# Performance work log

Hardware: AMD Instinct MI355X
Metric: run time of the kernel (lower is better)

Reference implementation:

```python
import jax, jax.numpy as jnp
import numpy as np

DIM = 128      # d_model (C)
DEPTH = 8
D_INNER = 2 * DIM      # expand=2
D_STATE = 16
D_CONV = 4
DT_RANK = (DIM + 15) // 16  # ceil(d_model/16) = 8
EPS = 1e-6
B_SZ, H_SZ, W_SZ = 2, 64, 64


def setup_inputs() -> dict:
    key = jax.random.key(0)
    ks = jax.random.split(key, 8)
    s = 0.02
    f32 = jnp.float32
    inp = {
        "x": jax.random.normal(ks[0], (B_SZ, DIM, H_SZ, W_SZ), f32),
        "in_proj_w": (jax.random.normal(ks[1], (DEPTH, 2 * D_INNER, DIM), f32) * s),
        "conv_w": (jax.random.normal(ks[2], (DEPTH, D_INNER, D_CONV), f32) * s),
        "conv_b": jnp.zeros((DEPTH, D_INNER), f32),
        "x_proj_w": (jax.random.normal(ks[3], (DEPTH, DT_RANK + 2 * D_STATE, D_INNER), f32) * s),
        "dt_proj_w": (jax.random.normal(ks[4], (DEPTH, D_INNER, DT_RANK), f32) * s),
        "dt_proj_b": jax.random.uniform(ks[5], (DEPTH, D_INNER), f32, -4.0, -2.0),
        "A_log": jnp.tile(jnp.log(jnp.arange(1.0, D_STATE + 1.0, dtype=f32))[None, None, :], (DEPTH, D_INNER, 1)),
        "D_skip": jnp.ones((DEPTH, D_INNER), f32),
        "out_proj_w": (jax.random.normal(ks[6], (DEPTH, DIM, D_INNER), f32) * s),
        "rms_w": jnp.ones((DIM,), f32),
    }
    return inp


def _selective_scan(u, delta, A, Bm, Cm, D_skip):
    # u, delta: [B,L,Dn]; A: [Dn,N]; Bm, Cm: [B,L,N]; D_skip: [Dn]
    dA = jnp.exp(delta[..., None] * A)                      # [B,L,Dn,N]
    dBu = (delta * u)[..., None] * Bm[:, :, None, :]        # [B,L,Dn,N]
    def comb(c1, c2):
        a1, b1 = c1
        a2, b2 = c2
        return a1 * a2, a2 * b1 + b2
    _, h = jax.lax.associative_scan(comb, (dA, dBu), axis=1)  # h: [B,L,Dn,N]
    y = jnp.einsum('bldn,bln->bld', h, Cm) + u * D_skip
    return y


def _mamba_layer(x, in_w, cw, cb, xp_w, dtw, dtb, A_log, D_skip, out_w):
    # x: [B,L,D]
    xz = jnp.einsum('bld,ed->ble', x, in_w)                 # [B,L,2*Dn]
    xin, z = jnp.split(xz, 2, axis=-1)
    # causal depthwise conv1d, kernel D_CONV, left-pad D_CONV-1
    lhs = jnp.transpose(xin, (0, 2, 1))                     # [B,Dn,L]
    rhs = cw[:, None, :]                                    # [Dn,1,K]
    xc = jax.lax.conv_general_dilated(
        lhs, rhs, window_strides=(1,), padding=[(D_CONV - 1, 0)],
        dimension_numbers=('NCH', 'OIH', 'NCH'), feature_group_count=D_INNER)
    xc = xc + cb[None, :, None]
    xc = jax.nn.silu(jnp.transpose(xc, (0, 2, 1)))          # [B,L,Dn]
    x_dbl = jnp.einsum('bld,ed->ble', xc, xp_w)             # [B,L,dt_rank+2N]
    dt, Bm, Cm = jnp.split(x_dbl, [DT_RANK, DT_RANK + D_STATE], axis=-1)
    delta = jax.nn.softplus(jnp.einsum('blr,dr->bld', dt, dtw) + dtb)
    A = -jnp.exp(A_log)                                     # [Dn,N]
    y = _selective_scan(xc, delta, A, Bm, Cm, D_skip)       # [B,L,Dn]
    y = y * jax.nn.silu(z)
    return jnp.einsum('bld,od->blo', y, out_w)              # [B,L,D]


def reference(x, in_proj_w, conv_w, conv_b, x_proj_w, dt_proj_w, dt_proj_b,
              A_log, D_skip, out_proj_w, rms_w):
    B, C, H, W = x.shape
    h = jnp.transpose(x.reshape(B, C, H * W), (0, 2, 1))    # [B,L,C]
    for i in range(DEPTH):
        h = _mamba_layer(h, in_proj_w[i], conv_w[i], conv_b[i], x_proj_w[i],
                         dt_proj_w[i], dt_proj_b[i], A_log[i], D_skip[i],
                         out_proj_w[i])
    # RMSNorm over channel dim
    h = h * jax.lax.rsqrt(jnp.mean(h * h, axis=-1, keepdims=True) + EPS) * rms_w
    return jnp.transpose(h.reshape(B, H, W, C), (0, 3, 1, 2))
```

## Files before the change

kernel.cpp:

```cpp
#include <hip/hip_runtime.h>
#include <math.h>

#define B_SZ   2
#define L_SEQ  4096
#define DIMC   128
#define DI     256
#define DST    16
#define DTR    8
#define NXP    40
#define NXPP   48
#define NLAYER 8
#define NCH    256
#define CS     16
#define LOG2E  1.4426950408889634f
#define LN2    0.6931471805599453f
#define PSA    264

#define N_INW  (NLAYER * 512 * 128)
#define N_XPW  (NLAYER * NXPP * DI)
#define N_OW   (NLAYER * DIMC * DI)
#define N_AF   (NLAYER * DI * DST)

typedef __attribute__((ext_vector_type(8))) unsigned short u16x8;
typedef __attribute__((ext_vector_type(4))) float f32x4;

__device__ __forceinline__ float fexp2(float x){ float r; asm("v_exp_f32 %0, %1" : "=v"(r) : "v"(x)); return r; }
__device__ __forceinline__ float flog2(float x){ float r; asm("v_log_f32 %0, %1" : "=v"(r) : "v"(x)); return r; }
__device__ __forceinline__ float frcp (float x){ float r; asm("v_rcp_f32 %0, %1" : "=v"(r) : "v"(x)); return r; }

__device__ __forceinline__ float silu_f(float x) {
    return x * frcp(1.f + fexp2(-x * LOG2E));
}
__device__ __forceinline__ float softplus_f(float x) {
    float t = fexp2(-fabsf(x) * LOG2E);
    return fmaxf(x, 0.f) + flog2(1.f + t) * LN2;
}
__device__ __forceinline__ void splitf(float x, unsigned short& h, unsigned short& l) {
    unsigned bx = __builtin_bit_cast(unsigned, x);
    h = (unsigned short)(bx >> 16);
    float fh = __builtin_bit_cast(float, bx & 0xffff0000u);
    float r = x - fh;
    l = (unsigned short)(__builtin_bit_cast(unsigned, r) >> 16);
}
__device__ __forceinline__ float bf2f(unsigned short u) {
    return __builtin_bit_cast(float, (unsigned)u << 16);
}

__global__ void prep(const float* __restrict__ in_w, const float* __restrict__ xp_w,
                     const float* __restrict__ out_w, const float* __restrict__ A_log,
                     unsigned short* __restrict__ iwh, unsigned short* __restrict__ iwl,
                     unsigned short* __restrict__ xpwh, unsigned short* __restrict__ xpwl,
                     unsigned short* __restrict__ owh, unsigned short* __restrict__ owl,
                     float* __restrict__ Af) {
    const int i = blockIdx.x * 256 + threadIdx.x;
    if (i < N_INW) { unsigned short h, l; splitf(in_w[i], h, l); iwh[i] = h; iwl[i] = l; }
    if (i < N_XPW) {
        int ly = i / (NXPP * DI), rem = i % (NXPP * DI);
        int c = rem / DI, k = rem % DI;
        unsigned short h = 0, l = 0;
        if (c < NXP) splitf(xp_w[((size_t)ly * NXP + c) * DI + k], h, l);
        xpwh[i] = h; xpwl[i] = l;
    }
    if (i < N_OW) { unsigned short h, l; splitf(out_w[i], h, l); owh[i] = h; owl[i] = l; }
    if (i < N_AF) Af[i] = -expf(A_log[i]) * LOG2E;
}

__global__ void transpose_in(const float* __restrict__ x, unsigned short* __restrict__ hh,
                             unsigned short* __restrict__ hl) {
    __shared__ float tl[32][33];
    const int b  = blockIdx.x;
    const int c0 = blockIdx.y * 32;
    const int l0 = blockIdx.z * 32;
    const int tx = threadIdx.x;
    const int ty = threadIdx.y;
    #pragma unroll
    for (int r = 0; r < 4; ++r) {
        int c = c0 + ty + r * 8;
        tl[ty + r * 8][tx] = x[((size_t)b * DIMC + c) * L_SEQ + l0 + tx];
    }
    __syncthreads();
    #pragma unroll
    for (int r = 0; r < 4; ++r) {
        int l = l0 + ty + r * 8;
        float v = tl[tx][ty + r * 8];
        size_t o = ((size_t)b * L_SEQ + l) * DIMC + c0 + tx;
        unsigned short h16, l16; splitf(v, h16, l16);
        hh[o] = h16; hl[o] = l16;
    }
}

template<int BM, int BN>
__global__ __launch_bounds__(256) void gemm_sp(
    const unsigned short* __restrict__ Ahg, const unsigned short* __restrict__ Alg,
    const unsigned short* __restrict__ Whg, const unsigned short* __restrict__ Wlg,
    float* __restrict__ C, int M, int N, int K) {
    constexpr int PS = 40;
    __shared__ unsigned short lds[(BM + BN) * 2 * PS];
    unsigned short* LAh = lds;
    unsigned short* LAl = LAh + BM * PS;
    unsigned short* LBh = LAl + BM * PS;
    unsigned short* LBl = LBh + BN * PS;
    const int t = threadIdx.x;
    const int w = t >> 6, l = t & 63;
    const int wr = w >> 1, wc = w & 1;
    const int lr = l & 15, lq = l >> 4;
    constexpr int MF = BM / 32, NF = BN / 32;
    const int bm = blockIdx.x * BM, bn = blockIdx.y * BN;
    f32x4 acc[MF][NF];
    const f32x4 z4 = {0.f, 0.f, 0.f, 0.f};
    #pragma unroll
    for (int m = 0; m < MF; ++m)
        #pragma unroll
        for (int n = 0; n < NF; ++n) acc[m][n] = z4;

    for (int k0 = 0; k0 < K; k0 += 32) {
        if (k0) __syncthreads();
        #pragma unroll
        for (int s = 0; s < BM * 4 / 256; ++s) {
            int task = t + s * 256;
            int r = task >> 2, g = task & 3;
            size_t go = (size_t)(bm + r) * K + k0 + g * 8;
            *(u16x8*)&LAh[r * PS + g * 8] = *(const u16x8*)&Ahg[go];
            *(u16x8*)&LAl[r * PS + g * 8] = *(const u16x8*)&Alg[go];
        }
        #pragma unroll
        for (int s = 0; s < BN * 4 / 256; ++s) {
            int task = t + s * 256;
            int r = task >> 2, g = task & 3;
            size_t go = (size_t)(bn + r) * K + k0 + g * 8;
            *(u16x8*)&LBh[r * PS + g * 8] = *(const u16x8*)&Whg[go];
            *(u16x8*)&LBl[r * PS + g * 8] = *(const u16x8*)&Wlg[go];
        }
        __syncthreads();
        u16x8 ah[MF], al[MF], bh[NF], bl[NF];
        #pragma unroll
        for (int m = 0; m < MF; ++m) {
            int rr = wr * (BM / 2) + m * 16 + lr;
            ah[m] = *(u16x8*)&LAh[rr * PS + lq * 8];
            al[m] = *(u16x8*)&LAl[rr * PS + lq * 8];
        }
        #pragma unroll
        for (int n = 0; n < NF; ++n) {
            int rr = wc * (BN / 2) + n * 16 + lr;
            bh[n] = *(u16x8*)&LBh[rr * PS + lq * 8];
            bl[n] = *(u16x8*)&LBl[rr * PS + lq * 8];
        }
        #pragma unroll
        for (int m = 0; m < MF; ++m)
            #pragma unroll
            for (int n = 0; n < NF; ++n) {
                asm("v_mfma_f32_16x16x32_bf16 %0, %1, %2, %0" : "+v"(acc[m][n]) : "v"(ah[m]), "v"(bh[n]));
                asm("v_mfma_f32_16x16x32_bf16 %0, %1, %2, %0" : "+v"(acc[m][n]) : "v"(ah[m]), "v"(bl[n]));
                asm("v_mfma_f32_16x16x32_bf16 %0, %1, %2, %0" : "+v"(acc[m][n]) : "v"(al[m]), "v"(bh[n]));
            }
    }
    #pragma unroll
    for (int m = 0; m < MF; ++m)
        #pragma unroll
        for (int n = 0; n < NF; ++n) {
            int col = bn + wc * (BN / 2) + n * 16 + lr;
            #pragma unroll
            for (int r = 0; r < 4; ++r) {
                int row = bm + wr * (BM / 2) + m * 16 + lq * 4 + r;
                C[(size_t)row * N + col] = acc[m][n][r];
            }
        }
}

__global__ __launch_bounds__(256) void fused_mid(
    const float* __restrict__ xz,
    const unsigned short* __restrict__ xpwh, const unsigned short* __restrict__ xpwl,
    const float* __restrict__ dtw, const float* __restrict__ dtb,
    const float* __restrict__ cw, const float* __restrict__ cb,
    const float* __restrict__ Af_g,
    float* __restrict__ xdbl, float* __restrict__ paO, float* __restrict__ hO) {
    const int ch = blockIdx.x & (NCH - 1);
    const int d  = threadIdx.x;
    const size_t r0 = (size_t)(blockIdx.x >> 8) * L_SEQ + ch * CS;
    __shared__ unsigned short aS[2][CS][PSA];
    __shared__ float P[4][CS][49];
    __shared__ float xdblS[CS][41];

    {
        const float w0 = cw[d * 4 + 0], w1 = cw[d * 4 + 1];
        const float w2 = cw[d * 4 + 2], w3 = cw[d * 4 + 3];
        const float bz = cb[d];
        float p0 = 0.f, p1 = 0.f, p2 = 0.f;
        if (ch > 0) {
            p0 = xz[(r0 - 3) * 512 + d];
            p1 = xz[(r0 - 2) * 512 + d];
            p2 = xz[(r0 - 1) * 512 + d];
        }
        #pragma unroll 4
        for (int i = 0; i < CS; ++i) {
            float cur = xz[(r0 + i) * 512 + d];
            float v = silu_f(fmaf(w3, cur, fmaf(w2, p2, fmaf(w1, p1, fmaf(w0, p0, bz)))));
            unsigned short h16, l16; splitf(v, h16, l16);
            aS[0][i][d] = h16; aS[1][i][d] = l16;
            p0 = p1; p1 = p2; p2 = cur;
        }
    }
    __syncthreads();

    const int w = threadIdx.x >> 6, l = threadIdx.x & 63;
    const int lr = l & 15, lq = l >> 4;
    {
        f32x4 acc[3];
        const f32x4 z4 = {0.f, 0.f, 0.f, 0.f};
        #pragma unroll
        for (int n = 0; n < 3; ++n) acc[n] = z4;
        #pragma unroll
        for (int ks = 0; ks < 2; ++ks) {
            const int kk = w * 64 + ks * 32 + lq * 8;
            u16x8 ah, al, bh[3], bl[3];
            ah = *(const u16x8*)&aS[0][lr][kk];
            al = *(const u16x8*)&aS[1][lr][kk];
            #pragma unroll
            for (int n = 0; n < 3; ++n) {
                const int c = n * 16 + lr;
                bh[n] = *(const u16x8*)&xpwh[c * DI + kk];
                bl[n] = *(const u16x8*)&xpwl[c * DI + kk];
            }
            #pragma unroll
            for (int n = 0; n < 3; ++n) {
                asm("v_mfma_f32_16x16x32_bf16 %0, %1, %2, %0" : "+v"(acc[n]) : "v"(ah), "v"(bh[n]));
                asm("v_mfma_f32_16x16x32_bf16 %0, %1, %2, %0" : "+v"(acc[n]) : "v"(ah), "v"(bl[n]));
                asm("v_mfma_f32_16x16x32_bf16 %0, %1, %2, %0" : "+v"(acc[n]) : "v"(al), "v"(bh[n]));
            }
        }
        #pragma unroll
        for (int n = 0; n < 3; ++n)
            #pragma unroll
            for (int r = 0; r < 4; ++r)
                P[w][lq * 4 + r][n * 16 + lr] = acc[n][r];
    }
    __syncthreads();
    {
        const int i = threadIdx.x >> 4;
        const int cb0 = threadIdx.x & 15;
        for (int c = cb0; c < NXP; c += 16) {
            float s = P[0][i][c] + P[1][i][c] + P[2][i][c] + P[3][i][c];
            xdblS[i][c] = s;
            xdbl[(r0 + i) * NXP + c] = s;
        }
    }
    __syncthreads();

    float wt[DTR];
    #pragma unroll
    for (int r = 0; r < DTR; ++r) wt[r] = dtw[d * DTR + r];
    const float bt = dtb[d];
    float Af[DST], h[DST], pa[DST];
    #pragma unroll
    for (int n = 0; n < DST; ++n) {
        Af[n] = Af_g[d * DST + n];
        h[n] = 0.f; pa[n] = 1.f;
    }
    #pragma unroll 4
    for (int i = 0; i < CS; ++i) {
        float s = bt;
        #pragma unroll
        for (int r = 0; r < DTR; ++r) s = fmaf(xdblS[i][r], wt[r], s);
        const float dl = softplus_f(s);
        const float u = bf2f(aS[0][i][d]) + bf2f(aS[1][i][d]);
        const float du = dl * u;
        #pragma unroll
        for (int n = 0; n < DST; ++n) {
            const float dA = fexp2(dl * Af[n]);
            pa[n] *= dA;
            h[n] = fmaf(dA, h[n], du * xdblS[i][DTR + n]);
        }
    }
    const size_t o = ((size_t)blockIdx.x * DI + d) * DST;
    #pragma unroll
    for (int n = 0; n < DST; ++n) { paO[o + n] = pa[n]; hO[o + n] = h[n]; }
}

__global__ void scan_combine(float* __restrict__ paO, const float* __restrict__ hO) {
    const int t  = blockIdx.x * 64 + threadIdx.x;
    const int b  = t / (DI * DST);
    const int dn = t % (DI * DST);
    float run = 0.f;
    for (int ch0 = 0; ch0 < NCH; ch0 += 8) {
        float pav[8], hv[8];
        #pragma unroll
        for (int j = 0; j < 8; ++j) {
            size_t o = ((size_t)(b * NCH + ch0 + j)) * DI * DST + dn;
            pav[j] = paO[o]; hv[j] = hO[o];
        }
        #pragma unroll
        for (int j = 0; j < 8; ++j) {
            size_t o = ((size_t)(b * NCH + ch0 + j)) * DI * DST + dn;
            paO[o] = run;
            run = fmaf(pav[j], run, hv[j]);
        }
    }
}

template<int LAST>
__global__ __launch_bounds__(256) void fused_out(
    const float* __restrict__ xz, const float* __restrict__ xdbl,
    const unsigned short* __restrict__ owh, const unsigned short* __restrict__ owl,
    const float* __restrict__ dtw, const float* __restrict__ dtb,
    const float* __restrict__ cw, const float* __restrict__ cb,
    const float* __restrict__ Af_g, const float* __restrict__ D_skip,
    const float* __restrict__ hinit,
    unsigned short* __restrict__ hh, unsigned short* __restrict__ hl,
    const float* __restrict__ rw, float* __restrict__ out) {
    __shared__ __align__(16) char smem[19520];
    unsigned short* ySh = (unsigned short*)smem;
    unsigned short* ySl = ySh + CS * PSA;
    float (*xdblS)[41] = (float (*)[41])(smem + 16896);
    const int ch = blockIdx.x & (NCH - 1);
    const int d  = threadIdx.x;
    const int b  = blockIdx.x >> 8;
    const size_t r0 = (size_t)b * L_SEQ + ch * CS;

    {
        const float* src = xdbl + r0 * NXP;
        for (int idx = threadIdx.x; idx < CS * NXP; idx += 256)
            xdblS[idx / NXP][idx % NXP] = src[idx];
    }
    float wt[DTR];
    #pragma unroll
    for (int r = 0; r < DTR; ++r) wt[r] = dtw[d * DTR + r];
    const float bt = dtb[d];
    const float Dd = D_skip[d];
    const float w0 = cw[d * 4 + 0], w1 = cw[d * 4 + 1];
    const float w2 = cw[d * 4 + 2], w3 = cw[d * 4 + 3];
    const float bz = cb[d];
    float Af[DST], h[DST];
    const size_t o = ((size_t)blockIdx.x * DI + d) * DST;
    #pragma unroll
    for (int n = 0; n < DST; ++n) {
        Af[n] = Af_g[d * DST + n];
        h[n] = hinit[o + n];
    }
    float p0 = 0.f, p1 = 0.f, p2 = 0.f;
    if (ch > 0) {
        p0 = xz[(r0 - 3) * 512 + d];
        p1 = xz[(r0 - 2) * 512 + d];
        p2 = xz[(r0 - 1) * 512 + d];
    }
    __syncthreads();

    #pragma unroll 4
    for (int i = 0; i < CS; ++i) {
        const float cur = xz[(r0 + i) * 512 + d];
        const float zv  = xz[(r0 + i) * 512 + DI + d];
        const float u = silu_f(fmaf(w3, cur, fmaf(w2, p2, fmaf(w1, p1, fmaf(w0, p0, bz)))));
        p0 = p1; p1 = p2; p2 = cur;
        float s = bt;
        #pragma unroll
        for (int r = 0; r < DTR; ++r) s = fmaf(xdblS[i][r], wt[r], s);
        const float dl = softplus_f(s);
        const float du = dl * u;
        float acc = 0.f;
        #pragma unroll
        for (int n = 0; n < DST; ++n) {
            const float dA = fexp2(dl * Af[n]);
            h[n] = fmaf(dA, h[n], du * xdblS[i][DTR + n]);
            acc = fmaf(h[n], xdblS[i][DTR + DST + n], acc);
        }
        const float y = (acc + u * Dd) * silu_f(zv);
        unsigned short h16, l16; splitf(y, h16, l16);
        ySh[i * PSA + d] = h16; ySl[i * PSA + d] = l16;
    }
    __syncthreads();

    const int w = threadIdx.x >> 6, l = threadIdx.x & 63;
    const int lr = l & 15, lq = l >> 4;
    f32x4 acc[2];
    const f32x4 z4 = {0.f, 0.f, 0.f, 0.f};
    #pragma unroll
    for (int n = 0; n < 2; ++n) acc[n] = z4;
    #pragma unroll
    for (int ks = 0; ks < 8; ++ks) {
        const int kk = ks * 32 + lq * 8;
        u16x8 ah = *(const u16x8*)&ySh[lr * PSA + kk];
        u16x8 al = *(const u16x8*)&ySl[lr * PSA + kk];
        #pragma unroll
        for (int n = 0; n < 2; ++n) {
            const int c = w * 32 + n * 16 + lr;
            u16x8 bh = *(const u16x8*)&owh[c * DI + kk];
            u16x8 bl = *(const u16x8*)&owl[c * DI + kk];
            asm("v_mfma_f32_16x16x32_bf16 %0, %1, %2, %0" : "+v"(acc[n]) : "v"(ah), "v"(bh));
            asm("v_mfma_f32_16x16x32_bf16 %0, %1, %2, %0" : "+v"(acc[n]) : "v"(ah), "v"(bl));
            asm("v_mfma_f32_16x16x32_bf16 %0, %1, %2, %0" : "+v"(acc[n]) : "v"(al), "v"(bh));
        }
    }

    if constexpr (!LAST) {
        #pragma unroll
        for (int n = 0; n < 2; ++n) {
            const int col = w * 32 + n * 16 + lr;
            #pragma unroll
            for (int r = 0; r < 4; ++r) {
                const size_t row = r0 + lq * 4 + r;
                unsigned short h16, l16; splitf(acc[n][r], h16, l16);
                hh[row * DIMC + col] = h16;
                hl[row * DIMC + col] = l16;
            }
        }
    } else {
        __syncthreads();
        float (*hS)[132] = (float (*)[132])smem;
        float* ps   = (float*)(smem + 8448);
        float* rinv = (float*)(smem + 8448 + 1024);
        #pragma unroll
        for (int n = 0; n < 2; ++n) {
            const int col = w * 32 + n * 16 + lr;
            #pragma unroll
            for (int r = 0; r < 4; ++r)
                hS[lq * 4 + r][col] = acc[n][r];
        }
        __syncthreads();
        {
            const int row = threadIdx.x >> 4, seg = threadIdx.x & 15;
            float s = 0.f;
            #pragma unroll
            for (int j = 0; j < 8; ++j) { float v = hS[row][seg * 8 + j]; s = fmaf(v, v, s); }
            ps[row * 16 + seg] = s;
        }
        __syncthreads();
        if (threadIdx.x < 16) {
            float s = 0.f;
            #pragma unroll
            for (int k = 0; k < 16; ++k) s += ps[threadIdx.x * 16 + k];
            rinv[threadIdx.x] = rsqrtf(s / DIMC + 1e-6f);
        }
        __syncthreads();
        {
            const int cc = threadIdx.x >> 1, half = threadIdx.x & 1;
            const float rwc = rw[cc];
            float v[8];
            #pragma unroll
            for (int j = 0; j < 8; ++j) {
                const int row = half * 8 + j;
                v[j] = hS[row][cc] * rinv[row] * rwc;
            }
            float* dst = out + ((size_t)b * DIMC + cc) * L_SEQ + ch * CS + half * 8;
            *(f32x4*)dst       = *(f32x4*)&v[0];
            *(f32x4*)(dst + 4) = *(f32x4*)&v[4];
        }
    }
}

extern "C" void kernel_launch(void* const* d_in, const int* in_sizes, int n_in,
                              void* d_out, int out_size, void* d_ws, size_t ws_size,
                              hipStream_t stream) {
    const float* x      = (const float*)d_in[0];
    const float* in_w   = (const float*)d_in[1];
    const float* conv_w = (const float*)d_in[2];
    const float* conv_b = (const float*)d_in[3];
    const float* xp_w   = (const float*)d_in[4];
    const float* dt_w   = (const float*)d_in[5];
    const float* dt_b   = (const float*)d_in[6];
    const float* A_log  = (const float*)d_in[7];
    const float* D_skip = (const float*)d_in[8];
    const float* out_w  = (const float*)d_in[9];
    const float* rms_w  = (const float*)d_in[10];
    float* out = (float*)d_out;

    const int M = B_SZ * L_SEQ;
    char* p = (char*)d_ws;
    auto alloc = [&](size_t bytes) -> void* {
        void* r = (void*)p; p += (bytes + 255) & ~(size_t)255; return r;
    };
    float* xz   = (float*)alloc((size_t)M * 512 * 4);
    float* xdbl = (float*)alloc((size_t)M * NXP * 4);
    float* paB  = (float*)alloc((size_t)B_SZ * NCH * DI * DST * 4);
    float* hB   = (float*)alloc((size_t)B_SZ * NCH * DI * DST * 4);
    float* AfT  = (float*)alloc((size_t)N_AF * 4);
    unsigned short* hh0 = (unsigned short*)alloc((size_t)M * DIMC * 2);
    unsigned short* hl0 = (unsigned short*)alloc((size_t)M * DIMC * 2);
    unsigned short* hh1 = (unsigned short*)alloc((size_t)M * DIMC * 2);
    unsigned short* hl1 = (unsigned short*)alloc((size_t)M * DIMC * 2);
    unsigned short* iwh = (unsigned short*)alloc((size_t)N_INW * 2);
    unsigned short* iwl = (unsigned short*)alloc((size_t)N_INW * 2);
    unsigned short* xpwh = (unsigned short*)alloc((size_t)N_XPW * 2);
    unsigned short* xpwl = (unsigned short*)alloc((size_t)N_XPW * 2);
    unsigned short* owh = (unsigned short*)alloc((size_t)N_OW * 2);
    unsigned short* owl = (unsigned short*)alloc((size_t)N_OW * 2);

    prep<<<(N_INW + 255) / 256, 256, 0, stream>>>(
        in_w, xp_w, out_w, A_log, iwh, iwl, xpwh, xpwl, owh, owl, AfT);

    transpose_in<<<dim3(B_SZ, DIMC / 32, L_SEQ / 32), dim3(32, 8), 0, stream>>>(x, hh0, hl0);

    unsigned short *hhin = hh0, *hlin = hl0, *hhout = hh1, *hlout = hl1;
    for (int layer = 0; layer < NLAYER; ++layer) {
        const float* cw  = conv_w + (size_t)layer * DI * 4;
        const float* cb  = conv_b + (size_t)layer * DI;
        const float* dtw = dt_w   + (size_t)layer * DI * DTR;
        const float* dtb = dt_b   + (size_t)layer * DI;
        const float* af  = AfT    + (size_t)layer * DI * DST;
        const float* ds  = D_skip + (size_t)layer * DI;
        const size_t iwo = (size_t)layer * 512 * 128;
        const size_t xpo = (size_t)layer * NXPP * DI;
        const size_t owo = (size_t)layer * DIMC * DI;

        gemm_sp<64, 128><<<dim3(M / 64, 4), 256, 0, stream>>>(
            hhin, hlin, iwh + iwo, iwl + iwo, xz, M, 512, 128);
        fused_mid<<<B_SZ * NCH, 256, 0, stream>>>(
            xz, xpwh + xpo, xpwl + xpo, dtw, dtb, cw, cb, af, xdbl, paB, hB);
        scan_combine<<<(B_SZ * DI * DST) / 64, 64, 0, stream>>>(paB, hB);
        if (layer < NLAYER - 1) {
            fused_out<0><<<B_SZ * NCH, 256, 0, stream>>>(
                xz, xdbl, owh + owo, owl + owo, dtw, dtb, cw, cb, af, ds, paB,
                hhout, hlout, nullptr, nullptr);
        } else {
            fused_out<1><<<B_SZ * NCH, 256, 0, stream>>>(
                xz, xdbl, owh + owo, owl + owo, dtw, dtb, cw, cb, af, ds, paB,
                nullptr, nullptr, rms_w, out);
        }

        unsigned short* ts;
        ts = hhin; hhin = hhout; hhout = ts;
        ts = hlin; hlin = hlout; hlout = ts;
    }
}
```

Before: 544.3 us.

## Double fused_mid block to 512 threads, splitting state dim and K across waves

Launches fused_mid with 512 threads. The second half of the block handles state indices 8-15 of the chunk scan, so each thread carries 8 states instead of 16. The x_proj MFMA K-loop is now spread over 8 waves with one K-step each, and the partial-sum reduction grows to 8 slices. The conv stage runs only on the first 256 threads. The goal is more parallelism and lower per-thread register use and latency in the serial scan loop, at the cost of extra shared memory, duplicated delta/softplus computation and idle threads during the conv stage.

Result: slower. 562.4 us (+3.3%).

```diff
diff --git a/kernel.cpp b/kernel.cpp
--- a/kernel.cpp
+++ b/kernel.cpp
@@ -167,7 +167,7 @@
         }
 }
 
-__global__ __launch_bounds__(256) void fused_mid(
+__global__ __launch_bounds__(512) void fused_mid(
     const float* __restrict__ xz,
     const unsigned short* __restrict__ xpwh, const unsigned short* __restrict__ xpwl,
     const float* __restrict__ dtw, const float* __restrict__ dtb,
@@ -175,13 +175,15 @@
     const float* __restrict__ Af_g,
     float* __restrict__ xdbl, float* __restrict__ paO, float* __restrict__ hO) {
     const int ch = blockIdx.x & (NCH - 1);
-    const int d  = threadIdx.x;
+    const int t  = threadIdx.x;
+    const int d  = t & 255;
+    const int sh = t >> 8;
     const size_t r0 = (size_t)(blockIdx.x >> 8) * L_SEQ + ch * CS;
     __shared__ unsigned short aS[2][CS][PSA];
-    __shared__ float P[4][CS][49];
+    __shared__ float P[8][CS][49];
     __shared__ float xdblS[CS][41];
 
-    {
+    if (sh == 0) {
         const float w0 = cw[d * 4 + 0], w1 = cw[d * 4 + 1];
         const float w2 = cw[d * 4 + 2], w3 = cw[d * 4 + 3];
         const float bz = cb[d];
@@ -202,31 +204,28 @@
     }
     __syncthreads();
 
-    const int w = threadIdx.x >> 6, l = threadIdx.x & 63;
+    const int w = t >> 6, l = t & 63;
     const int lr = l & 15, lq = l >> 4;
     {
         f32x4 acc[3];
         const f32x4 z4 = {0.f, 0.f, 0.f, 0.f};
         #pragma unroll
         for (int n = 0; n < 3; ++n) acc[n] = z4;
-        #pragma unroll
-        for (int ks = 0; ks < 2; ++ks) {
-            const int kk = w * 64 + ks * 32 + lq * 8;
-            u16x8 ah, al, bh[3], bl[3];
-            ah = *(const u16x8*)&aS[0][lr][kk];
-            al = *(const u16x8*)&aS[1][lr][kk];
-            #pragma unroll
-            for (int n = 0; n < 3; ++n) {
-                const int c = n * 16 + lr;
-                bh[n] = *(const u16x8*)&xpwh[c * DI + kk];
-                bl[n] = *(const u16x8*)&xpwl[c * DI + kk];
-            }
-            #pragma unroll
-            for (int n = 0; n < 3; ++n) {
-                asm("v_mfma_f32_16x16x32_bf16 %0, %1, %2, %0" : "+v"(acc[n]) : "v"(ah), "v"(bh[n]));
-                asm("v_mfma_f32_16x16x32_bf16 %0, %1, %2, %0" : "+v"(acc[n]) : "v"(ah), "v"(bl[n]));
-                asm("v_mfma_f32_16x16x32_bf16 %0, %1, %2, %0" : "+v"(acc[n]) : "v"(al), "v"(bh[n]));
-            }
+        const int kk = w * 32 + lq * 8;
+        u16x8 ah, al, bh[3], bl[3];
+        ah = *(const u16x8*)&aS[0][lr][kk];
+        al = *(const u16x8*)&aS[1][lr][kk];
+        #pragma unroll
+        for (int n = 0; n < 3; ++n) {
+            const int c = n * 16 + lr;
+            bh[n] = *(const u16x8*)&xpwh[c * DI + kk];
+            bl[n] = *(const u16x8*)&xpwl[c * DI + kk];
+        }
+        #pragma unroll
+        for (int n = 0; n < 3; ++n) {
+            asm("v_mfma_f32_16x16x32_bf16 %0, %1, %2, %0" : "+v"(acc[n]) : "v"(ah), "v"(bh[n]));
+            asm("v_mfma_f32_16x16x32_bf16 %0, %1, %2, %0" : "+v"(acc[n]) : "v"(ah), "v"(bl[n]));
+            asm("v_mfma_f32_16x16x32_bf16 %0, %1, %2, %0" : "+v"(acc[n]) : "v"(al), "v"(bh[n]));
         }
         #pragma unroll
         for (int n = 0; n < 3; ++n)
@@ -236,12 +235,20 @@
     }
     __syncthreads();
     {
-        const int i = threadIdx.x >> 4;
-        const int cb0 = threadIdx.x & 15;
-        for (int c = cb0; c < NXP; c += 16) {
-            float s = P[0][i][c] + P[1][i][c] + P[2][i][c] + P[3][i][c];
-            xdblS[i][c] = s;
-            xdbl[(r0 + i) * NXP + c] = s;
+        const int i = t >> 5;
+        const int cb = t & 31;
+        {
+            float s = P[0][i][cb] + P[1][i][cb] + P[2][i][cb] + P[3][i][cb]
+                    + P[4][i][cb] + P[5][i][cb] + P[6][i][cb] + P[7][i][cb];
+            xdblS[i][cb] = s;
+            xdbl[(r0 + i) * NXP + cb] = s;
+        }
+        if (cb < 8) {
+            const int c2 = cb + 32;
+            float s = P[0][i][c2] + P[1][i][c2] + P[2][i][c2] + P[3][i][c2]
+                    + P[4][i][c2] + P[5][i][c2] + P[6][i][c2] + P[7][i][c2];
+            xdblS[i][c2] = s;
+            xdbl[(r0 + i) * NXP + c2] = s;
         }
     }
     __syncthreads();
@@ -250,10 +257,10 @@
     #pragma unroll
     for (int r = 0; r < DTR; ++r) wt[r] = dtw[d * DTR + r];
     const float bt = dtb[d];
-    float Af[DST], h[DST], pa[DST];
-    #pragma unroll
-    for (int n = 0; n < DST; ++n) {
-        Af[n] = Af_g[d * DST + n];
+    float Af[8], h[8], pa[8];
+    #pragma unroll
+    for (int n = 0; n < 8; ++n) {
+        Af[n] = Af_g[d * DST + sh * 8 + n];
         h[n] = 0.f; pa[n] = 1.f;
     }
     #pragma unroll 4
@@ -265,15 +272,15 @@
         const float u = bf2f(aS[0][i][d]) + bf2f(aS[1][i][d]);
         const float du = dl * u;
         #pragma unroll
-        for (int n = 0; n < DST; ++n) {
+        for (int n = 0; n < 8; ++n) {
             const float dA = fexp2(dl * Af[n]);
             pa[n] *= dA;
-            h[n] = fmaf(dA, h[n], du * xdblS[i][DTR + n]);
-        }
-    }
-    const size_t o = ((size_t)blockIdx.x * DI + d) * DST;
-    #pragma unroll
-    for (int n = 0; n < DST; ++n) { paO[o + n] = pa[n]; hO[o + n] = h[n]; }
+            h[n] = fmaf(dA, h[n], du * xdblS[i][DTR + sh * 8 + n]);
+        }
+    }
+    const size_t o = ((size_t)blockIdx.x * DI + d) * DST + sh * 8;
+    #pragma unroll
+    for (int n = 0; n < 8; ++n) { paO[o + n] = pa[n]; hO[o + n] = h[n]; }
 }
 
 __global__ void scan_combine(float* __restrict__ paO, const float* __restrict__ hO) {
@@ -502,7 +509,7 @@
 
         gemm_sp<64, 128><<<dim3(M / 64, 4), 256, 0, stream>>>(
             hhin, hlin, iwh + iwo, iwl + iwo, xz, M, 512, 128);
-        fused_mid<<<B_SZ * NCH, 256, 0, stream>>>(
+        fused_mid<<<B_SZ * NCH, 512, 0, stream>>>(
             xz, xpwh + xpo, xpwl + xpo, dtw, dtb, cw, cb, af, xdbl, paB, hB);
         scan_combine<<<(B_SZ * DI * DST) / 64, 64, 0, stream>>>(paB, hB);
         if (layer < NLAYER - 1) {
```
